# Optimization experiments

Hardware: AMD Instinct MI355X
Metric: run time of the kernel (lower is better)

Reference implementation:

```python
import jax, jax.numpy as jnp
from jax import lax
import numpy as np

# ---- geometry constants (from metadata / module __init__) ----
NA = 1152            # rotview (number of projection angles)
ND = 736             # det_count
NP = 512             # reconstructed image size
VOX = 1.0 / 0.7      # vox_scaling
D   = VOX * 595.0    # source-to-isocenter distance
DD  = VOX * 490.6    # isocenter-to-detector distance
DU  = VOX * 1.2858   # detector pixel spacing
DSD = D + DD         # source-to-detector distance
ANGLES = np.linspace(0.0, 2.0 * np.pi, NA, endpoint=False) + np.pi / 2.0

# ---- Shepp-Logan Fourier filter (skimage/torch-radon construction) ----
PAD = max(64, int(2 ** np.ceil(np.log2(2 * ND))))  # 2048

def _shepp_logan_filter(size):
    n = np.concatenate([np.arange(1, size // 2 + 1, 2),
                        np.arange(size // 2 - 1, 0, -2)])
    f = np.zeros(size)
    f[0] = 0.25
    f[1::2] = -1.0 / (np.pi * n) ** 2
    four = 2.0 * np.real(np.fft.fft(f))            # ramp filter
    omega = np.pi * np.fft.fftfreq(size)[1:]
    four[1:] *= np.sin(omega) / omega              # Shepp-Logan window
    return four[: size // 2 + 1].astype(np.float32)  # rfft half-spectrum

FILT = jnp.asarray(_shepp_logan_filter(PAD))
COS_A = jnp.asarray(np.cos(ANGLES).astype(np.float32))
SIN_A = jnp.asarray(np.sin(ANGLES).astype(np.float32))


def _filter_sinogram(sino):
    # sino: (NA, ND). Zero-pad to PAD, filter in Fourier domain, crop.
    padded = jnp.pad(sino, ((0, 0), (0, PAD - ND)))
    spec = jnp.fft.rfft(padded, axis=-1) * FILT
    filt = jnp.fft.irfft(spec, n=PAD, axis=-1)[:, :ND]
    return filt * (np.pi / (2.0 * NA))


def _backproject(filtered):
    # Pixel-driven fan-beam (flat detector) backprojection.
    c = (NP - 1) / 2.0
    coords = jnp.arange(NP, dtype=jnp.float32) - c
    ys, xs = jnp.meshgrid(coords, coords, indexing='ij')  # (NP, NP)

    def body(acc, inp):
        cb, sb, row = inp
        pdot = xs * cb + ys * sb            # pixel coord along source dir
        pe = -xs * sb + ys * cb             # pixel coord along detector axis
        den = D - pdot                      # source->pixel depth
        u = DSD * pe / den                  # detector coordinate (mm)
        iu = u / DU + (ND - 1) / 2.0        # fractional detector index
        i0 = jnp.floor(iu)
        frac = iu - i0
        i0i = i0.astype(jnp.int32)
        valid = (i0i >= 0) & (i0i < ND - 1) & (den > 0)
        i0c = jnp.clip(i0i, 0, ND - 2)
        v = row[i0c] * (1.0 - frac) + row[i0c + 1] * frac  # linear interp
        w = (D / den) ** 2                   # fan-beam distance weighting
        return acc + jnp.where(valid, w * v, 0.0), None

    img, _ = lax.scan(body, jnp.zeros((NP, NP), jnp.float32),
                      (COS_A, SIN_A, filtered))
    return img


def setup_inputs() -> dict:
    key = jax.random.key(0)
    x = jax.random.normal(key, (1, 1, NA, ND), dtype=jnp.float32)
    return {"x": x}


def reference(x):
    sino = x[0, 0]                          # (NA, ND) after squeeze
    filtered = _filter_sinogram(sino)
    fbp = _backproject(filtered)
    # mu -> HU -> normalize to [0, 1] window
    fbp_hu = (1000.0 * ((fbp - 0.0192) / 0.0192) - (-1024.0)) / (3072.0 - (-1024.0))
    return fbp_hu[None, None]               # (1, 1, 512, 512)
```

## Files before the change

### kernel.cpp

```cpp
#include <hip/hip_runtime.h>
#include <math.h>

#ifndef M_PI
#define M_PI 3.14159265358979323846
#endif

#define NAANG 1152
#define NDET  736
#define NPIX  512
#define PADN  2048
#define NHALF 1025

#define OFF_COST  0
#define OFF_FILTF 8192
#define OFF_H     12416
#define OFF_TRIG  20608
#define OFF_FS    39040
#define OFF_PART  3430528

typedef int int32x4_t __attribute__((ext_vector_type(4)));
__device__ float llvm_amdgcn_struct_buffer_load_fp32(int32x4_t srsrc,
                                                     int vindex, int voffset,
                                                     int soffset, int cachepolicy)
    __asm("llvm.amdgcn.struct.buffer.load.f32");

__global__ void costab_kernel(float* __restrict__ cosT) {
    int r = blockIdx.x * 256 + threadIdx.x;
    cosT[r] = (float)cos(2.0 * M_PI * (double)r / (double)PADN);
}

__global__ void filt_spec_kernel(const float* __restrict__ cosT,
                                 float* __restrict__ filt_f) {
    __shared__ float red[256];
    const int m = blockIdx.x;
    const int t = threadIdx.x;
    float s = 0.f;
    for (int j = t; j < 1024; j += 256) {
        int n = (j < 512) ? (2 * j + 1) : (2047 - 2 * j);
        float fj = (float)(-1.0 / ((M_PI * n) * (M_PI * n)));
        s += fj * cosT[(m * (2 * j + 1)) & (PADN - 1)];
    }
    red[t] = s;
    __syncthreads();
    for (int w = 128; w > 0; w >>= 1) {
        if (t < w) red[t] += red[t + w];
        __syncthreads();
    }
    if (t == 0) {
        double four = 2.0 * (0.25 + (double)red[0]);
        if (m > 0) {
            double om = M_PI * (double)m / (double)PADN;
            four *= sin(om) / om;
        }
        filt_f[m] = (float)four;
    }
}

__global__ void h_kernel(const float* __restrict__ cosT,
                         const float* __restrict__ filt_f,
                         float* __restrict__ h, float4* __restrict__ trig) {
    __shared__ float red[256];
    const int k = blockIdx.x;
    const int t = threadIdx.x;
    if (t == 0 && k < NAANG) {
        double ang = 2.0 * M_PI * (double)k / (double)NAANG + M_PI / 2.0;
        double c = cos(ang), s = sin(ang);
        double K = 1085.6 / 1.2858;
        trig[k] = make_float4((float)c, (float)s, (float)(K * c), (float)(K * s));
    }
    float s = 0.f;
    for (int m = t; m <= 1024; m += 256) {
        float F = filt_f[m];
        float c;
        if (m == 0) c = 1.f;
        else if (m == 1024) c = (k & 1) ? -1.f : 1.f;
        else c = 2.f * cosT[(m * k) & (PADN - 1)];
        s += F * c;
    }
    red[t] = s;
    __syncthreads();
    for (int w = 128; w > 0; w >>= 1) {
        if (t < w) red[t] += red[t + w];
        __syncthreads();
    }
    if (t == 0)
        h[k] = (float)((double)red[0] / (double)PADN * (M_PI / (2.0 * (double)NAANG)));
}

__global__ void conv_kernel(const float* __restrict__ x,
                            const float* __restrict__ h,
                            float* __restrict__ fs) {
    __shared__ float sh2[2816];
    __shared__ float srow[NDET];
    const int row = blockIdx.x;
    const int t = threadIdx.x;
    const float4* h4 = (const float4*)h;
    for (int i = t; i < 704; i += 192) ((float4*)sh2)[i] = h4[i & 511];
    const float4* x4 = (const float4*)(x + row * NDET);
    for (int i = t; i < NDET / 4; i += 192) ((float4*)srow)[i] = x4[i];
    __syncthreads();

    const int t4 = 4 * t;
    float o0 = 0.f, o1 = 0.f, o2 = 0.f, o3 = 0.f;
    #pragma unroll 2
    for (int j = 0; j < NDET; j += 4) {
        float4 r4 = *(const float4*)&srow[j];
        const int A = t4 + PADN - j;
        float4 hlo = *(const float4*)&sh2[A - 4];
        float4 hhi = *(const float4*)&sh2[A];
        o0 = fmaf(r4.x, hhi.x, o0); o0 = fmaf(r4.y, hlo.w, o0);
        o0 = fmaf(r4.z, hlo.z, o0); o0 = fmaf(r4.w, hlo.y, o0);
        o1 = fmaf(r4.x, hhi.y, o1); o1 = fmaf(r4.y, hhi.x, o1);
        o1 = fmaf(r4.z, hlo.w, o1); o1 = fmaf(r4.w, hlo.z, o1);
        o2 = fmaf(r4.x, hhi.z, o2); o2 = fmaf(r4.y, hhi.y, o2);
        o2 = fmaf(r4.z, hhi.x, o2); o2 = fmaf(r4.w, hlo.w, o2);
        o3 = fmaf(r4.x, hhi.w, o3); o3 = fmaf(r4.y, hhi.z, o3);
        o3 = fmaf(r4.z, hhi.y, o3); o3 = fmaf(r4.w, hhi.x, o3);
    }
    if (t < NDET / 4)
        *(float4*)&fs[row * NDET + t4] = make_float4(o0, o1, o2, o3);
}

#define GEO(AA, G0L,G0H,G1L,G1H,G2L,G2H,G3L,G3H, FR0,FR1,FR2,FR3, W0,W1,W2,W3) \
  {                                                                      \
    float4 q = trig[abase + (AA)];           \
    const float* rp_ = fs + (size_t)(abase + (AA)) * NDET;               \
    uintptr_t ua_ = (uintptr_t)rp_;                                      \
    int32x4_t sA_ = { (int)ua_, (int)(ua_ >> 32) | 0x00040000, 735,      \
                      0x00020000 };                                      \
    uintptr_t ub_ = ua_ + 4;                                             \
    int32x4_t sB_ = { (int)ub_, (int)(ub_ >> 32) | 0x00040000, 735,      \
                      0x00020000 };                                      \
    float den0 = fmaf(-xs, q.x, fmaf(-ys0, q.y, Dg));                    \
    float kpe0 = fmaf(ys0, q.z, -(xs * q.w));                            \
    float den1 = den0 - q.y, den2 = den1 - q.y, den3 = den2 - q.y;       \
    float kpe1 = kpe0 + q.z, kpe2 = kpe1 + q.z, kpe3 = kpe2 + q.z;       \
    float r0 = __builtin_amdgcn_rcpf(den0);                              \
    float r1 = __builtin_amdgcn_rcpf(den1);                              \
    float r2 = __builtin_amdgcn_rcpf(den2);                              \
    float r3 = __builtin_amdgcn_rcpf(den3);                              \
    float iu0 = fmaf(kpe0, r0, 367.5f);                                  \
    float iu1 = fmaf(kpe1, r1, 367.5f);                                  \
    float iu2 = fmaf(kpe2, r2, 367.5f);                                  \
    float iu3 = fmaf(kpe3, r3, 367.5f);                                  \
    int i0 = (int)floorf(iu0);                                           \
    int i1 = (int)floorf(iu1);                                           \
    int i2 = (int)floorf(iu2);                                           \
    int i3 = (int)floorf(iu3);                                           \
    asm("v_fract_f32 %0, %1" : "=v"(FR0) : "v"(iu0));                    \
    asm("v_fract_f32 %0, %1" : "=v"(FR1) : "v"(iu1));                    \
    asm("v_fract_f32 %0, %1" : "=v"(FR2) : "v"(iu2));                    \
    asm("v_fract_f32 %0, %1" : "=v"(FR3) : "v"(iu3));                    \
    G0L = llvm_amdgcn_struct_buffer_load_fp32(sA_, i0, 0, 0, 0);         \
    G0H = llvm_amdgcn_struct_buffer_load_fp32(sB_, i0, 0, 0, 0);         \
    G1L = llvm_amdgcn_struct_buffer_load_fp32(sA_, i1, 0, 0, 0);         \
    G1H = llvm_amdgcn_struct_buffer_load_fp32(sB_, i1, 0, 0, 0);         \
    G2L = llvm_amdgcn_struct_buffer_load_fp32(sA_, i2, 0, 0, 0);         \
    G2H = llvm_amdgcn_struct_buffer_load_fp32(sB_, i2, 0, 0, 0);         \
    G3L = llvm_amdgcn_struct_buffer_load_fp32(sA_, i3, 0, 0, 0);         \
    G3H = llvm_amdgcn_struct_buffer_load_fp32(sB_, i3, 0, 0, 0);         \
    W0 = r0 * r0; W1 = r1 * r1; W2 = r2 * r2; W3 = r3 * r3;              \
  }

#define CONSUME(G0L,G0H,G1L,G1H,G2L,G2H,G3L,G3H, FR0,FR1,FR2,FR3, W0,W1,W2,W3) \
  {                                                                      \
    float v0 = fmaf(FR0, G0H - G0L, G0L);                                \
    float v1 = fmaf(FR1, G1H - G1L, G1L);                                \
    float v2 = fmaf(FR2, G2H - G2L, G2L);                                \
    float v3 = fmaf(FR3, G3H - G3L, G3L);                                \
    acc0 = fmaf(W0, v0, acc0); acc1 = fmaf(W1, v1, acc1);                \
    acc2 = fmaf(W2, v2, acc2); acc3 = fmaf(W3, v3, acc3);                \
  }

template<int NCH>
__global__ __launch_bounds__(256, 8)
void backproj_kernel(const float* __restrict__ fs,
                     const float4* __restrict__ trig,
                     float* __restrict__ partial) {
    constexpr int ACL = NAANG / NCH;
    const int t = threadIdx.x;
    const int abase = blockIdx.z * ACL;
    const int ix = blockIdx.x * 256 + t;
    const int iy = blockIdx.y * 4;
    const float xs  = (float)ix - 255.5f;
    const float ys0 = (float)iy - 255.5f;
    const float Dg = 850.0f;

    float acc0 = 0.f, acc1 = 0.f, acc2 = 0.f, acc3 = 0.f;
    float Ag0l, Ag0h, Ag1l, Ag1h, Ag2l, Ag2h, Ag3l, Ag3h;
    float Bg0l, Bg0h, Bg1l, Bg1h, Bg2l, Bg2h, Bg3l, Bg3h;
    float Af0, Af1, Af2, Af3, Aw0, Aw1, Aw2, Aw3;
    float Bf0, Bf1, Bf2, Bf3, Bw0, Bw1, Bw2, Bw3;

    GEO(0, Ag0l,Ag0h,Ag1l,Ag1h,Ag2l,Ag2h,Ag3l,Ag3h, Af0,Af1,Af2,Af3, Aw0,Aw1,Aw2,Aw3);
    int a = 0;
    for (; a + 2 < ACL; a += 2) {
        GEO(a + 1, Bg0l,Bg0h,Bg1l,Bg1h,Bg2l,Bg2h,Bg3l,Bg3h, Bf0,Bf1,Bf2,Bf3, Bw0,Bw1,Bw2,Bw3);
        CONSUME(Ag0l,Ag0h,Ag1l,Ag1h,Ag2l,Ag2h,Ag3l,Ag3h, Af0,Af1,Af2,Af3, Aw0,Aw1,Aw2,Aw3);
        GEO(a + 2, Ag0l,Ag0h,Ag1l,Ag1h,Ag2l,Ag2h,Ag3l,Ag3h, Af0,Af1,Af2,Af3, Aw0,Aw1,Aw2,Aw3);
        CONSUME(Bg0l,Bg0h,Bg1l,Bg1h,Bg2l,Bg2h,Bg3l,Bg3h, Bf0,Bf1,Bf2,Bf3, Bw0,Bw1,Bw2,Bw3);
    }
    GEO(ACL - 1, Bg0l,Bg0h,Bg1l,Bg1h,Bg2l,Bg2h,Bg3l,Bg3h, Bf0,Bf1,Bf2,Bf3, Bw0,Bw1,Bw2,Bw3);
    CONSUME(Ag0l,Ag0h,Ag1l,Ag1h,Ag2l,Ag2h,Ag3l,Ag3h, Af0,Af1,Af2,Af3, Aw0,Aw1,Aw2,Aw3);
    CONSUME(Bg0l,Bg0h,Bg1l,Bg1h,Bg2l,Bg2h,Bg3l,Bg3h, Bf0,Bf1,Bf2,Bf3, Bw0,Bw1,Bw2,Bw3);

    float* outp = partial + ((size_t)blockIdx.z * NPIX + iy) * NPIX + ix;
    outp[0 * NPIX] = acc0;
    outp[1 * NPIX] = acc1;
    outp[2 * NPIX] = acc2;
    outp[3 * NPIX] = acc3;
}

template<int NCH>
__global__ void combine_kernel(const float* __restrict__ partial,
                               float* __restrict__ out) {
    int p = blockIdx.x * 256 + threadIdx.x;
    float s = 0.f;
    #pragma unroll
    for (int c = 0; c < NCH; ++c) s += partial[c * NPIX * NPIX + p];
    out[p] = fmaf(s, (float)(722500.0 * 1000.0 / 0.0192 / 4096.0), 0.005859375f);
}

extern "C" void kernel_launch(void* const* d_in, const int* in_sizes, int n_in,
                              void* d_out, int out_size, void* d_ws, size_t ws_size,
                              hipStream_t stream) {
    const float* x = (const float*)d_in[0];
    float* out = (float*)d_out;

    char* ws = (char*)d_ws;
    float*  cosT   = (float*)(ws + OFF_COST);
    float*  filt_f = (float*)(ws + OFF_FILTF);
    float*  h      = (float*)(ws + OFF_H);
    float4* trig   = (float4*)(ws + OFF_TRIG);
    float*  fs     = (float*)(ws + OFF_FS);
    float*  part   = (float*)(ws + OFF_PART);

    costab_kernel<<<PADN / 256, 256, 0, stream>>>(cosT);
    filt_spec_kernel<<<NHALF, 256, 0, stream>>>(cosT, filt_f);
    h_kernel<<<PADN, 256, 0, stream>>>(cosT, filt_f, h, trig);
    conv_kernel<<<NAANG, 192, 0, stream>>>(x, h, fs);

    const size_t pbytes = (size_t)NPIX * NPIX * 4;
    if (ws_size >= OFF_PART + 16 * pbytes) {
        backproj_kernel<16><<<dim3(2, 128, 16), 256, 0, stream>>>(fs, trig, part);
        combine_kernel<16><<<NPIX * NPIX / 256, 256, 0, stream>>>(part, out);
    } else if (ws_size >= OFF_PART + 8 * pbytes) {
        backproj_kernel<8><<<dim3(2, 128, 8), 256, 0, stream>>>(fs, trig, part);
        combine_kernel<8><<<NPIX * NPIX / 256, 256, 0, stream>>>(part, out);
    } else if (ws_size >= OFF_PART + 4 * pbytes) {
        backproj_kernel<4><<<dim3(2, 128, 4), 256, 0, stream>>>(fs, trig, part);
        combine_kernel<4><<<NPIX * NPIX / 256, 256, 0, stream>>>(part, out);
    } else if (ws_size >= OFF_PART + 2 * pbytes) {
        backproj_kernel<2><<<dim3(2, 128, 2), 256, 0, stream>>>(fs, trig, part);
        combine_kernel<2><<<NPIX * NPIX / 256, 256, 0, stream>>>(part, out);
    } else {
        backproj_kernel<1><<<dim3(2, 128, 1), 256, 0, stream>>>(fs, trig, part);
        combine_kernel<1><<<NPIX * NPIX / 256, 256, 0, stream>>>(part, out);
    }
}
```

Before: 242.8 us.

## Deepen backprojection gather pipeline to three stages and cap angle chunks at 8

The backprojection loop now keeps three angle sets (A/B/C) in flight instead of two, so the buffer-load gathers for two future angles overlap with consuming the current one. To make room for the extra live registers, the launch-bounds occupancy hint drops from 8 to 6 waves per SIMD. The 16-chunk angle split is removed, so the largest configuration is 8 chunks, which gives fewer blocks and a cheaper combine pass. The trade-off is lower occupancy and less grid parallelism in exchange for more memory-level parallelism per thread.

After: 248.1 us. 2.2% more time.

```diff
diff --git a/kernel.cpp b/kernel.cpp
--- a/kernel.cpp
+++ b/kernel.cpp
@@ -121,7 +121,7 @@
         *(float4*)&fs[row * NDET + t4] = make_float4(o0, o1, o2, o3);
 }
 
-#define GEO(AA, G0L,G0H,G1L,G1H,G2L,G2H,G3L,G3H, FR0,FR1,FR2,FR3, W0,W1,W2,W3) \
+#define GEO(AA, S)                                                       \
   {                                                                      \
     float4 q = trig[abase + (AA)];           \
     const float* rp_ = fs + (size_t)(abase + (AA)) * NDET;               \
@@ -147,37 +147,42 @@
     int i1 = (int)floorf(iu1);                                           \
     int i2 = (int)floorf(iu2);                                           \
     int i3 = (int)floorf(iu3);                                           \
-    asm("v_fract_f32 %0, %1" : "=v"(FR0) : "v"(iu0));                    \
-    asm("v_fract_f32 %0, %1" : "=v"(FR1) : "v"(iu1));                    \
-    asm("v_fract_f32 %0, %1" : "=v"(FR2) : "v"(iu2));                    \
-    asm("v_fract_f32 %0, %1" : "=v"(FR3) : "v"(iu3));                    \
-    G0L = llvm_amdgcn_struct_buffer_load_fp32(sA_, i0, 0, 0, 0);         \
-    G0H = llvm_amdgcn_struct_buffer_load_fp32(sB_, i0, 0, 0, 0);         \
-    G1L = llvm_amdgcn_struct_buffer_load_fp32(sA_, i1, 0, 0, 0);         \
-    G1H = llvm_amdgcn_struct_buffer_load_fp32(sB_, i1, 0, 0, 0);         \
-    G2L = llvm_amdgcn_struct_buffer_load_fp32(sA_, i2, 0, 0, 0);         \
-    G2H = llvm_amdgcn_struct_buffer_load_fp32(sB_, i2, 0, 0, 0);         \
-    G3L = llvm_amdgcn_struct_buffer_load_fp32(sA_, i3, 0, 0, 0);         \
-    G3H = llvm_amdgcn_struct_buffer_load_fp32(sB_, i3, 0, 0, 0);         \
-    W0 = r0 * r0; W1 = r1 * r1; W2 = r2 * r2; W3 = r3 * r3;              \
+    asm("v_fract_f32 %0, %1" : "=v"(S##f0) : "v"(iu0));                  \
+    asm("v_fract_f32 %0, %1" : "=v"(S##f1) : "v"(iu1));                  \
+    asm("v_fract_f32 %0, %1" : "=v"(S##f2) : "v"(iu2));                  \
+    asm("v_fract_f32 %0, %1" : "=v"(S##f3) : "v"(iu3));                  \
+    S##g0l = llvm_amdgcn_struct_buffer_load_fp32(sA_, i0, 0, 0, 0);      \
+    S##g0h = llvm_amdgcn_struct_buffer_load_fp32(sB_, i0, 0, 0, 0);      \
+    S##g1l = llvm_amdgcn_struct_buffer_load_fp32(sA_, i1, 0, 0, 0);      \
+    S##g1h = llvm_amdgcn_struct_buffer_load_fp32(sB_, i1, 0, 0, 0);      \
+    S##g2l = llvm_amdgcn_struct_buffer_load_fp32(sA_, i2, 0, 0, 0);      \
+    S##g2h = llvm_amdgcn_struct_buffer_load_fp32(sB_, i2, 0, 0, 0);      \
+    S##g3l = llvm_amdgcn_struct_buffer_load_fp32(sA_, i3, 0, 0, 0);      \
+    S##g3h = llvm_amdgcn_struct_buffer_load_fp32(sB_, i3, 0, 0, 0);      \
+    S##w0 = r0 * r0; S##w1 = r1 * r1; S##w2 = r2 * r2; S##w3 = r3 * r3;  \
   }
 
-#define CONSUME(G0L,G0H,G1L,G1H,G2L,G2H,G3L,G3H, FR0,FR1,FR2,FR3, W0,W1,W2,W3) \
+#define CONSUME(S)                                                       \
   {                                                                      \
-    float v0 = fmaf(FR0, G0H - G0L, G0L);                                \
-    float v1 = fmaf(FR1, G1H - G1L, G1L);                                \
-    float v2 = fmaf(FR2, G2H - G2L, G2L);                                \
-    float v3 = fmaf(FR3, G3H - G3L, G3L);                                \
-    acc0 = fmaf(W0, v0, acc0); acc1 = fmaf(W1, v1, acc1);                \
-    acc2 = fmaf(W2, v2, acc2); acc3 = fmaf(W3, v3, acc3);                \
+    float v0 = fmaf(S##f0, S##g0h - S##g0l, S##g0l);                     \
+    float v1 = fmaf(S##f1, S##g1h - S##g1l, S##g1l);                     \
+    float v2 = fmaf(S##f2, S##g2h - S##g2l, S##g2l);                     \
+    float v3 = fmaf(S##f3, S##g3h - S##g3l, S##g3l);                     \
+    acc0 = fmaf(S##w0, v0, acc0); acc1 = fmaf(S##w1, v1, acc1);          \
+    acc2 = fmaf(S##w2, v2, acc2); acc3 = fmaf(S##w3, v3, acc3);          \
   }
 
+#define DECLSET(S)                                                       \
+    float S##g0l, S##g0h, S##g1l, S##g1h, S##g2l, S##g2h, S##g3l, S##g3h;\
+    float S##f0, S##f1, S##f2, S##f3, S##w0, S##w1, S##w2, S##w3;
+
 template<int NCH>
-__global__ __launch_bounds__(256, 8)
+__global__ __launch_bounds__(256, 6)
 void backproj_kernel(const float* __restrict__ fs,
                      const float4* __restrict__ trig,
                      float* __restrict__ partial) {
     constexpr int ACL = NAANG / NCH;
+    static_assert(ACL % 3 == 0, "pipeline tail assumes ACL divisible by 3");
     const int t = threadIdx.x;
     const int abase = blockIdx.z * ACL;
     const int ix = blockIdx.x * 256 + t;
@@ -187,22 +192,18 @@
     const float Dg = 850.0f;
 
     float acc0 = 0.f, acc1 = 0.f, acc2 = 0.f, acc3 = 0.f;
-    float Ag0l, Ag0h, Ag1l, Ag1h, Ag2l, Ag2h, Ag3l, Ag3h;
-    float Bg0l, Bg0h, Bg1l, Bg1h, Bg2l, Bg2h, Bg3l, Bg3h;
-    float Af0, Af1, Af2, Af3, Aw0, Aw1, Aw2, Aw3;
-    float Bf0, Bf1, Bf2, Bf3, Bw0, Bw1, Bw2, Bw3;
-
-    GEO(0, Ag0l,Ag0h,Ag1l,Ag1h,Ag2l,Ag2h,Ag3l,Ag3h, Af0,Af1,Af2,Af3, Aw0,Aw1,Aw2,Aw3);
+    DECLSET(A) DECLSET(B) DECLSET(C)
+
+    GEO(0, A);
+    GEO(1, B);
     int a = 0;
-    for (; a + 2 < ACL; a += 2) {
-        GEO(a + 1, Bg0l,Bg0h,Bg1l,Bg1h,Bg2l,Bg2h,Bg3l,Bg3h, Bf0,Bf1,Bf2,Bf3, Bw0,Bw1,Bw2,Bw3);
-        CONSUME(Ag0l,Ag0h,Ag1l,Ag1h,Ag2l,Ag2h,Ag3l,Ag3h, Af0,Af1,Af2,Af3, Aw0,Aw1,Aw2,Aw3);
-        GEO(a + 2, Ag0l,Ag0h,Ag1l,Ag1h,Ag2l,Ag2h,Ag3l,Ag3h, Af0,Af1,Af2,Af3, Aw0,Aw1,Aw2,Aw3);
-        CONSUME(Bg0l,Bg0h,Bg1l,Bg1h,Bg2l,Bg2h,Bg3l,Bg3h, Bf0,Bf1,Bf2,Bf3, Bw0,Bw1,Bw2,Bw3);
-    }
-    GEO(ACL - 1, Bg0l,Bg0h,Bg1l,Bg1h,Bg2l,Bg2h,Bg3l,Bg3h, Bf0,Bf1,Bf2,Bf3, Bw0,Bw1,Bw2,Bw3);
-    CONSUME(Ag0l,Ag0h,Ag1l,Ag1h,Ag2l,Ag2h,Ag3l,Ag3h, Af0,Af1,Af2,Af3, Aw0,Aw1,Aw2,Aw3);
-    CONSUME(Bg0l,Bg0h,Bg1l,Bg1h,Bg2l,Bg2h,Bg3l,Bg3h, Bf0,Bf1,Bf2,Bf3, Bw0,Bw1,Bw2,Bw3);
+    for (; a + 5 < ACL; a += 3) {
+        GEO(a + 2, C); CONSUME(A);
+        GEO(a + 3, A); CONSUME(B);
+        GEO(a + 4, B); CONSUME(C);
+    }
+    GEO(a + 2, C);
+    CONSUME(A); CONSUME(B); CONSUME(C);
 
     float* outp = partial + ((size_t)blockIdx.z * NPIX + iy) * NPIX + ix;
     outp[0 * NPIX] = acc0;
@@ -241,10 +242,7 @@
     conv_kernel<<<NAANG, 192, 0, stream>>>(x, h, fs);
 
     const size_t pbytes = (size_t)NPIX * NPIX * 4;
-    if (ws_size >= OFF_PART + 16 * pbytes) {
-        backproj_kernel<16><<<dim3(2, 128, 16), 256, 0, stream>>>(fs, trig, part);
-        combine_kernel<16><<<NPIX * NPIX / 256, 256, 0, stream>>>(part, out);
-    } else if (ws_size >= OFF_PART + 8 * pbytes) {
+    if (ws_size >= OFF_PART + 8 * pbytes) {
         backproj_kernel<8><<<dim3(2, 128, 8), 256, 0, stream>>>(fs, trig, part);
         combine_kernel<8><<<NPIX * NPIX / 256, 256, 0, stream>>>(part, out);
     } else if (ws_size >= OFF_PART + 4 * pbytes) {
```
